# Optimization experiments

Hardware: AMD Instinct MI355X
Metric: run time of the kernel (lower is better)

Reference implementation:

```python
import jax, jax.numpy as jnp
import numpy as np

B, D, LC, LQ = 64, 128, 1024, 128
NEG = -1e30


def setup_inputs() -> dict:
    key = jax.random.key(0)
    k1, k2, k3 = jax.random.split(key, 3)
    lim = float(np.sqrt(1.0 / D))
    return {
        "C": jax.random.normal(k1, (B, D, LC), dtype=jnp.float32),
        "Q": jax.random.normal(k2, (B, D, LQ), dtype=jnp.float32),
        "cmask": jnp.ones((B, LC), dtype=jnp.float32),
        "qmask": jnp.ones((B, LQ), dtype=jnp.float32),
        "w": jax.random.uniform(k3, (3 * D,), dtype=jnp.float32, minval=-lim, maxval=lim),
    }


def reference(C, Q, cmask, qmask, w):
    # C: [B, D, Lc], Q: [B, D, Lq] -> transpose to [B, L, D] as in the torch module
    Ct = jnp.swapaxes(C, 1, 2)  # [B, Lc, D]
    Qt = jnp.swapaxes(Q, 1, 2)  # [B, Lq, D]
    d = Ct.shape[-1]
    # Trilinear decomposition of the per-step concat([Qi, C, Q*C]) . w loop:
    # S[b,c,q] = Qt[b,q] . w_q + Ct[b,c] . w_c + (Ct[b,c] * w_m) . Qt[b,q]
    w_q, w_c, w_m = w[:d], w[d:2 * d], w[2 * d:]
    s_q = Qt @ w_q                                   # [B, Lq]
    s_c = Ct @ w_c                                   # [B, Lc]
    s_m = jnp.einsum("bcd,bqd->bcq", Ct * w_m, Qt)   # [B, Lc, Lq]
    S = s_m + s_c[:, :, None] + s_q[:, None, :]      # [B, Lc, Lq]

    S1 = jax.nn.softmax(S + (1.0 - qmask)[:, None, :] * NEG, axis=2)
    S2 = jax.nn.softmax(S + (1.0 - cmask)[:, :, None] * NEG, axis=1)

    A = jnp.einsum("bcq,bqd->bcd", S1, Qt)           # [B, Lc, D]
    S12 = jnp.einsum("bcq,bkq->bck", S1, S2)         # [B, Lc, Lc]
    Bt = jnp.einsum("bck,bkd->bcd", S12, Ct)         # [B, Lc, D]

    out = jnp.concatenate([Ct, A, Ct * A, Ct * Bt], axis=2)  # [B, Lc, 4D]
    # dropout is identity in eval mode
    return jnp.swapaxes(out, 1, 2)                   # [B, 4D, Lc]
```

## Files before the change

kernel.cpp:

```cpp
#include <hip/hip_runtime.h>
#include <cstdint>
#include <cstddef>

#define B_  64
#define D_  128
#define LC_ 1024
#define LQ_ 128
#define NEGV (-1e30f)
#define NINF (-3.402823466e38f)

typedef short s16x8 __attribute__((ext_vector_type(8)));
typedef float f32x4 __attribute__((ext_vector_type(4)));

__device__ __forceinline__ unsigned short f2bf(float x) {
    union { float f; unsigned u; } v; v.f = x;
    unsigned r = v.u + 0x7fffu + ((v.u >> 16) & 1u);
    return (unsigned short)(r >> 16);
}
__device__ __forceinline__ float bf2f(unsigned short u) {
    union { unsigned u; float f; } v; v.u = ((unsigned)u) << 16; return v.f;
}

__global__ __launch_bounds__(256, 2) void k1(const float* __restrict__ C,
                                             const float* __restrict__ Q,
                                             const float* __restrict__ cmask,
                                             const float* __restrict__ qmask,
                                             const float* __restrict__ w,
                                             unsigned short* __restrict__ S1b,
                                             float* __restrict__ pmax_g,
                                             float* __restrict__ psum_g,
                                             unsigned short* __restrict__ T2pb) {
    __shared__ unsigned short CW[128 * 136];
    __shared__ unsigned short QT[128 * 136];
    __shared__ float4 red4[8][32];
    __shared__ float wc_l[128], wm_l[128], cmv_l[128], qmv_l[128], sc_l[128], sq_l[128];

    int t = threadIdx.x;
    int b = blockIdx.y, ct = blockIdx.x, c0 = ct * 128;
    int g = t >> 5, c4 = t & 31;

    float4 v[16];
    {
        const float4* Cb = (const float4*)(C + (size_t)b * D_ * LC_ + c0);
#pragma unroll
        for (int j = 0; j < 16; j++) {
            int d = j * 8 + g;
            v[j] = Cb[(size_t)d * (LC_ / 4) + c4];
        }
    }
    float* wq_l = (float*)red4;
    if (t < 128) {
        wq_l[t] = w[t];
        wc_l[t] = w[D_ + t];
        wm_l[t] = w[2 * D_ + t];
        cmv_l[t] = (1.0f - cmask[b * LC_ + c0 + t]) * NEGV;
        qmv_l[t] = (1.0f - qmask[b * LQ_ + t]) * NEGV;
    }
    __syncthreads();

    {
        float* CWf = (float*)CW;
        int qq = t >> 1, ph = t & 1;
        float sqv = 0.f;
#pragma unroll
        for (int h = 0; h < 2; h++) {
#pragma unroll
            for (int j = 0; j < 8; j++) {
                int idx = j * 256 + t;
                int r = idx >> 5, cc = idx & 31;
                float4 qv = *(const float4*)&Q[((size_t)(b * D_ + h * 64 + r)) * LQ_ + cc * 4];
                *(float4*)&CWf[r * 132 + cc * 4] = qv;
            }
            __syncthreads();
            unsigned short u[32];
#pragma unroll
            for (int k = 0; k < 32; k++) {
                float val = CWf[(ph * 32 + k) * 132 + qq];
                sqv += val * wq_l[h * 64 + ph * 32 + k];
                u[k] = f2bf(val);
            }
#pragma unroll
            for (int k4 = 0; k4 < 8; k4++) {
                ushort4 o;
                o.x = u[k4 * 4 + 0]; o.y = u[k4 * 4 + 1];
                o.z = u[k4 * 4 + 2]; o.w = u[k4 * 4 + 3];
                *(ushort4*)&QT[qq * 136 + h * 64 + ph * 32 + k4 * 4] = o;
            }
            __syncthreads();
        }
        sqv += __shfl_xor(sqv, 1, 64);
        if (ph == 0) sq_l[qq] = sqv;
    }

    {
        float4 scp = {0.f, 0.f, 0.f, 0.f};
#pragma unroll
        for (int j = 0; j < 16; j++) {
            int d = j * 8 + g;
            float wcv = wc_l[d], wmv = wm_l[d];
            scp.x += v[j].x * wcv;
            scp.y += v[j].y * wcv;
            scp.z += v[j].z * wcv;
            scp.w += v[j].w * wcv;
            ushort4 o;
            o.x = f2bf(v[j].x * wmv);
            o.y = f2bf(v[j].y * wmv);
            o.z = f2bf(v[j].z * wmv);
            o.w = f2bf(v[j].w * wmv);
            *(ushort4*)&CW[d * 136 + ((c4 ^ (j & 7)) << 2)] = o;
        }
        red4[g][c4] = scp;
    }
    __syncthreads();
    if (t < 128) {
        float s = 0.f;
#pragma unroll
        for (int gg = 0; gg < 8; gg++) {
            const float* rp = (const float*)&red4[gg][t >> 2];
            s += rp[t & 3];
        }
        sc_l[t] = s;
    }
    __syncthreads();

    int wv = t >> 6, l = t & 63, quad = l >> 4, lp = l & 15;
    int w32 = wv * 32;
    f32x4 zero = {0.f, 0.f, 0.f, 0.f};
    f32x4 acc[2][8];
#pragma unroll
    for (int mc = 0; mc < 2; mc++)
#pragma unroll
        for (int qt = 0; qt < 8; qt++) acc[mc][qt] = zero;

#pragma unroll
    for (int ks = 0; ks < 4; ks++) {
        s16x8 a[2], bb[8];
        int x3 = (ks * 4 + quad) & 7;
#pragma unroll
        for (int mc = 0; mc < 2; mc++) {
            s16x8 av;
            int c = w32 + mc * 16 + lp;
            int cb = ((c >> 2) ^ x3) << 2, clo = c & 3;
#pragma unroll
            for (int e = 0; e < 8; e++)
                av[e] = (short)CW[(ks * 32 + quad * 8 + e) * 136 + cb + clo];
            a[mc] = av;
        }
#pragma unroll
        for (int qt = 0; qt < 8; qt++)
            bb[qt] = *(const s16x8*)&QT[(qt * 16 + lp) * 136 + ks * 32 + quad * 8];
#pragma unroll
        for (int mc = 0; mc < 2; mc++)
#pragma unroll
            for (int qt = 0; qt < 8; qt++)
                acc[mc][qt] = __builtin_amdgcn_mfma_f32_16x16x32_bf16(a[mc], bb[qt], acc[mc][qt], 0, 0, 0);
    }
#pragma unroll
    for (int mc = 0; mc < 2; mc++)
#pragma unroll
        for (int qt = 0; qt < 8; qt++)
#pragma unroll
            for (int i = 0; i < 4; i++)
                acc[mc][qt][i] += sc_l[w32 + mc * 16 + quad * 4 + i] + sq_l[qt * 16 + lp];

    float qmv_r[8];
#pragma unroll
    for (int qt = 0; qt < 8; qt++) qmv_r[qt] = qmv_l[qt * 16 + lp];
    float cmv_r[2][4];
#pragma unroll
    for (int mc = 0; mc < 2; mc++)
#pragma unroll
        for (int i = 0; i < 4; i++) cmv_r[mc][i] = cmv_l[w32 + mc * 16 + quad * 4 + i];

    float rm_r[2][4];
#pragma unroll
    for (int mc = 0; mc < 2; mc++)
#pragma unroll
        for (int i = 0; i < 4; i++) {
            float m = NINF;
#pragma unroll
            for (int qt = 0; qt < 8; qt++) m = fmaxf(m, acc[mc][qt][i] + qmv_r[qt]);
#pragma unroll
            for (int off = 1; off < 16; off <<= 1) m = fmaxf(m, __shfl_xor(m, off, 64));
            rm_r[mc][i] = m;
        }

    int chunk = ct * 4 + wv;
#pragma unroll
    for (int qt = 0; qt < 8; qt++) {
        float cm = NINF;
#pragma unroll
        for (int mc = 0; mc < 2; mc++)
#pragma unroll
            for (int i = 0; i < 4; i++) cm = fmaxf(cm, acc[mc][qt][i] + cmv_r[mc][i]);
        cm = fmaxf(cm, __shfl_xor(cm, 16, 64));
        cm = fmaxf(cm, __shfl_xor(cm, 32, 64));
        float cs = 0.f;
#pragma unroll
        for (int mc = 0; mc < 2; mc++)
#pragma unroll
            for (int i = 0; i < 4; i++) cs += __expf(acc[mc][qt][i] + cmv_r[mc][i] - cm);
        cs += __shfl_xor(cs, 16, 64);
        cs += __shfl_xor(cs, 32, 64);
        if (l < 16) {
            pmax_g[((size_t)(b * 32 + chunk)) * LQ_ + qt * 16 + lp] = cm;
            psum_g[((size_t)(b * 32 + chunk)) * LQ_ + qt * 16 + lp] = cs;
        }
    }

    float ri_r[2][4], gs_r[2][4];
#pragma unroll
    for (int mc = 0; mc < 2; mc++)
#pragma unroll
        for (int i = 0; i < 4; i++) {
            float s = 0.f;
#pragma unroll
            for (int qt = 0; qt < 8; qt++) {
                float e = __expf(acc[mc][qt][i] + qmv_r[qt] - rm_r[mc][i]);
                acc[mc][qt][i] = e;
                s += e;
            }
#pragma unroll
            for (int off = 1; off < 16; off <<= 1) s += __shfl_xor(s, off, 64);
            ri_r[mc][i] = 1.0f / s;
            gs_r[mc][i] = s * __expf(rm_r[mc][i] + cmv_r[mc][i]);
        }

    __syncthreads();
#pragma unroll
    for (int mc = 0; mc < 2; mc++)
#pragma unroll
        for (int qt = 0; qt < 8; qt++)
#pragma unroll
            for (int i = 0; i < 4; i++) {
                int row = w32 + mc * 16 + quad * 4 + i;
                int q = qt * 16 + lp;
                float s1 = acc[mc][qt][i] * ri_r[mc][i];
                CW[row * 136 + q] = f2bf(s1);
                QT[q * 136 + row] = f2bf(s1 * gs_r[mc][i]);
            }
    __syncthreads();

    {
        int row = t >> 1, qh = (t & 1) * 64;
        const uint4* src = (const uint4*)&CW[row * 136 + qh];
        uint4* dst = (uint4*)&S1b[((size_t)(b * LC_ + c0 + row)) * LQ_ + qh];
#pragma unroll
        for (int j = 0; j < 8; j++) dst[j] = src[j];
    }

    f32x4 acc2[2][8];
#pragma unroll
    for (int mc = 0; mc < 2; mc++)
#pragma unroll
        for (int nt = 0; nt < 8; nt++) acc2[mc][nt] = zero;
#pragma unroll
    for (int ks = 0; ks < 4; ks++) {
        s16x8 a2[2], bb[8];
#pragma unroll
        for (int m = 0; m < 2; m++) {
            int d = w32 + m * 16 + lp;
            const float4* p = (const float4*)&C[((size_t)(b * D_ + d)) * LC_ + c0 + ks * 32 + quad * 8];
            float4 v0 = p[0], v1 = p[1];
            unsigned short* pp = (unsigned short*)&a2[m];
            pp[0] = f2bf(v0.x); pp[1] = f2bf(v0.y); pp[2] = f2bf(v0.z); pp[3] = f2bf(v0.w);
            pp[4] = f2bf(v1.x); pp[5] = f2bf(v1.y); pp[6] = f2bf(v1.z); pp[7] = f2bf(v1.w);
        }
#pragma unroll
        for (int nt = 0; nt < 8; nt++)
            bb[nt] = *(const s16x8*)&QT[(nt * 16 + lp) * 136 + ks * 32 + quad * 8];
#pragma unroll
        for (int m = 0; m < 2; m++)
#pragma unroll
            for (int nt = 0; nt < 8; nt++)
                acc2[m][nt] = __builtin_amdgcn_mfma_f32_16x16x32_bf16(a2[m], bb[nt], acc2[m][nt], 0, 0, 0);
    }
    size_t base = ((size_t)(ct * B_ + b)) * ((size_t)D_ * LQ_);
#pragma unroll
    for (int mc = 0; mc < 2; mc++)
#pragma unroll
        for (int i = 0; i < 4; i++) {
            int d = w32 + mc * 16 + quad * 4 + i;
#pragma unroll
            for (int nt = 0; nt < 8; nt++)
                T2pb[base + (size_t)d * LQ_ + nt * 16 + lp] = f2bf(acc2[mc][nt][i]);
        }
}

__global__ __launch_bounds__(256) void k2(const float* __restrict__ pmax_g,
                                          const float* __restrict__ psum_g,
                                          const unsigned short* __restrict__ T2pb,
                                          unsigned short* __restrict__ T2b) {
    __shared__ float scale_l[128];
    int t = threadIdx.x;
    int bid = blockIdx.x;
    int b = bid >> 3, dc = bid & 7;
    if (t < 128) {
        float m = NINF;
        for (int j = 0; j < 32; j++)
            m = fmaxf(m, pmax_g[((size_t)(b * 32 + j)) * LQ_ + t]);
        float s = 0.f;
        for (int j = 0; j < 32; j++)
            s += psum_g[((size_t)(b * 32 + j)) * LQ_ + t] *
                 __expf(pmax_g[((size_t)(b * 32 + j)) * LQ_ + t] - m);
        scale_l[t] = __expf(-m) / s;
    }
    __syncthreads();
    int d = dc * 16 + (t >> 4), q8 = (t & 15) * 8;
    float a8[8] = {0.f, 0.f, 0.f, 0.f, 0.f, 0.f, 0.f, 0.f};
#pragma unroll
    for (int j = 0; j < 8; j++) {
        const ushort4* p = (const ushort4*)&T2pb[(((size_t)j * B_ + b) * D_ + d) * LQ_ + q8];
        ushort4 x0 = p[0], x1 = p[1];
        a8[0] += bf2f(x0.x); a8[1] += bf2f(x0.y); a8[2] += bf2f(x0.z); a8[3] += bf2f(x0.w);
        a8[4] += bf2f(x1.x); a8[5] += bf2f(x1.y); a8[6] += bf2f(x1.z); a8[7] += bf2f(x1.w);
    }
    ushort4 o0, o1;
    o0.x = f2bf(a8[0] * scale_l[q8 + 0]);
    o0.y = f2bf(a8[1] * scale_l[q8 + 1]);
    o0.z = f2bf(a8[2] * scale_l[q8 + 2]);
    o0.w = f2bf(a8[3] * scale_l[q8 + 3]);
    o1.x = f2bf(a8[4] * scale_l[q8 + 4]);
    o1.y = f2bf(a8[5] * scale_l[q8 + 5]);
    o1.z = f2bf(a8[6] * scale_l[q8 + 6]);
    o1.w = f2bf(a8[7] * scale_l[q8 + 7]);
    size_t tb = ((size_t)(b * D_ + d)) * LQ_ + q8;
    *(ushort4*)&T2b[tb] = o0;
    *(ushort4*)&T2b[tb + 4] = o1;
}

__global__ __launch_bounds__(256) void k3(const float* __restrict__ C,
                                          const float* __restrict__ Q,
                                          const unsigned short* __restrict__ T2b,
                                          const unsigned short* __restrict__ S1b,
                                          float* __restrict__ out) {
    int t = threadIdx.x;
    int b = blockIdx.y, c0 = blockIdx.x * 128;
    int wv = t >> 6, l = t & 63, quad = l >> 4, lp = l & 15;
    int w32 = wv * 32;
    f32x4 zero = {0.f, 0.f, 0.f, 0.f};
    f32x4 accA[2][8], accB[2][8];
#pragma unroll
    for (int mc = 0; mc < 2; mc++)
#pragma unroll
        for (int nt = 0; nt < 8; nt++) { accA[mc][nt] = zero; accB[mc][nt] = zero; }

#pragma unroll
    for (int ks = 0; ks < 4; ks++) {
        s16x8 aq[2], at[2], bb[8];
#pragma unroll
        for (int mc = 0; mc < 2; mc++) {
            int d = w32 + mc * 16 + lp;
            const float4* p = (const float4*)&Q[((size_t)(b * D_ + d)) * LQ_ + ks * 32 + quad * 8];
            float4 v0 = p[0], v1 = p[1];
            unsigned short* pp = (unsigned short*)&aq[mc];
            pp[0] = f2bf(v0.x); pp[1] = f2bf(v0.y); pp[2] = f2bf(v0.z); pp[3] = f2bf(v0.w);
            pp[4] = f2bf(v1.x); pp[5] = f2bf(v1.y); pp[6] = f2bf(v1.z); pp[7] = f2bf(v1.w);
            at[mc] = *(const s16x8*)&T2b[((size_t)(b * D_ + d)) * LQ_ + ks * 32 + quad * 8];
        }
#pragma unroll
        for (int nt = 0; nt < 8; nt++)
            bb[nt] = *(const s16x8*)&S1b[((size_t)(b * LC_ + c0 + nt * 16 + lp)) * LQ_ + ks * 32 + quad * 8];
#pragma unroll
        for (int mc = 0; mc < 2; mc++)
#pragma unroll
            for (int nt = 0; nt < 8; nt++) {
                accA[mc][nt] = __builtin_amdgcn_mfma_f32_16x16x32_bf16(aq[mc], bb[nt], accA[mc][nt], 0, 0, 0);
                accB[mc][nt] = __builtin_amdgcn_mfma_f32_16x16x32_bf16(at[mc], bb[nt], accB[mc][nt], 0, 0, 0);
            }
    }
    const size_t DL = (size_t)D_ * LC_;
#pragma unroll
    for (int mc = 0; mc < 2; mc++)
#pragma unroll
        for (int i = 0; i < 4; i++) {
            int d = w32 + mc * 16 + quad * 4 + i;
            const float* Crow = C + ((size_t)(b * D_ + d)) * LC_ + c0;
            size_t ob = ((size_t)(b * 4 * D_ + d)) * LC_ + c0;
#pragma unroll
            for (int nt = 0; nt < 8; nt++) {
                int c = nt * 16 + lp;
                float cv = Crow[c];
                float a = accA[mc][nt][i];
                float bt = accB[mc][nt][i];
                out[ob + c] = cv;
                out[ob + DL + c] = a;
                out[ob + 2 * DL + c] = cv * a;
                out[ob + 3 * DL + c] = cv * bt;
            }
        }
}

extern "C" void kernel_launch(void* const* d_in, const int* in_sizes, int n_in,
                              void* d_out, int out_size, void* d_ws, size_t ws_size,
                              hipStream_t stream) {
    const float* C     = (const float*)d_in[0];
    const float* Q     = (const float*)d_in[1];
    const float* cmask = (const float*)d_in[2];
    const float* qmask = (const float*)d_in[3];
    const float* w     = (const float*)d_in[4];
    float* out = (float*)d_out;

    unsigned short* us = (unsigned short*)d_ws;
    unsigned short* S1b  = us;
    unsigned short* T2b  = S1b + (size_t)B_ * LC_ * LQ_;
    unsigned short* T2pb = T2b + (size_t)B_ * D_ * LQ_;
    float* fp = (float*)(T2pb + (size_t)8 * B_ * D_ * LQ_);
    float* pmax_g = fp;
    float* psum_g = pmax_g + (size_t)B_ * 32 * LQ_;

    k1<<<dim3(LC_ / 128, B_), 256, 0, stream>>>(C, Q, cmask, qmask, w,
                                                S1b, pmax_g, psum_g, T2pb);
    k2<<<dim3(B_ * 8), 256, 0, stream>>>(pmax_g, psum_g, T2pb, T2b);
    k3<<<dim3(LC_ / 128, B_), 256, 0, stream>>>(C, Q, T2b, S1b, out);
}
```

Baseline: 215.5 us.

## Fuse partial-T2 reduction kernel into output kernel via shared memory

Removes the separate k2 launch that reduced the eight partial T2 tiles and wrote a normalized bf16 T2 to global memory. Each k3 block now recomputes the column softmax scale and the full 128x128 T2 reduction for its batch into a padded LDS tile, then reads MFMA operands from LDS. This saves one launch and a global write/read round trip, but repeats the reduction eight times per batch (once per c-tile block). It also adds about 35 KB of LDS per block, which may lower occupancy.

```diff
diff --git a/kernel.cpp b/kernel.cpp
--- a/kernel.cpp
+++ b/kernel.cpp
@@ -287,14 +287,18 @@
         }
 }
 
-__global__ __launch_bounds__(256) void k2(const float* __restrict__ pmax_g,
+__global__ __launch_bounds__(256) void k3(const float* __restrict__ C,
+                                          const float* __restrict__ Q,
+                                          const float* __restrict__ pmax_g,
                                           const float* __restrict__ psum_g,
                                           const unsigned short* __restrict__ T2pb,
-                                          unsigned short* __restrict__ T2b) {
+                                          const unsigned short* __restrict__ S1b,
+                                          float* __restrict__ out) {
+    __shared__ unsigned short T2L[128 * 136];
     __shared__ float scale_l[128];
     int t = threadIdx.x;
-    int bid = blockIdx.x;
-    int b = bid >> 3, dc = bid & 7;
+    int b = blockIdx.y, c0 = blockIdx.x * 128;
+
     if (t < 128) {
         float m = NINF;
         for (int j = 0; j < 32; j++)
@@ -306,36 +310,34 @@
         scale_l[t] = __expf(-m) / s;
     }
     __syncthreads();
-    int d = dc * 16 + (t >> 4), q8 = (t & 15) * 8;
-    float a8[8] = {0.f, 0.f, 0.f, 0.f, 0.f, 0.f, 0.f, 0.f};
-#pragma unroll
-    for (int j = 0; j < 8; j++) {
-        const ushort4* p = (const ushort4*)&T2pb[(((size_t)j * B_ + b) * D_ + d) * LQ_ + q8];
-        ushort4 x0 = p[0], x1 = p[1];
-        a8[0] += bf2f(x0.x); a8[1] += bf2f(x0.y); a8[2] += bf2f(x0.z); a8[3] += bf2f(x0.w);
-        a8[4] += bf2f(x1.x); a8[5] += bf2f(x1.y); a8[6] += bf2f(x1.z); a8[7] += bf2f(x1.w);
-    }
-    ushort4 o0, o1;
-    o0.x = f2bf(a8[0] * scale_l[q8 + 0]);
-    o0.y = f2bf(a8[1] * scale_l[q8 + 1]);
-    o0.z = f2bf(a8[2] * scale_l[q8 + 2]);
-    o0.w = f2bf(a8[3] * scale_l[q8 + 3]);
-    o1.x = f2bf(a8[4] * scale_l[q8 + 4]);
-    o1.y = f2bf(a8[5] * scale_l[q8 + 5]);
-    o1.z = f2bf(a8[6] * scale_l[q8 + 6]);
-    o1.w = f2bf(a8[7] * scale_l[q8 + 7]);
-    size_t tb = ((size_t)(b * D_ + d)) * LQ_ + q8;
-    *(ushort4*)&T2b[tb] = o0;
-    *(ushort4*)&T2b[tb + 4] = o1;
-}
-
-__global__ __launch_bounds__(256) void k3(const float* __restrict__ C,
-                                          const float* __restrict__ Q,
-                                          const unsigned short* __restrict__ T2b,
-                                          const unsigned short* __restrict__ S1b,
-                                          float* __restrict__ out) {
-    int t = threadIdx.x;
-    int b = blockIdx.y, c0 = blockIdx.x * 128;
+
+    {
+        int dl = t >> 4, q0 = (t & 15) * 8;
+        float sc[8];
+#pragma unroll
+        for (int k = 0; k < 8; k++) sc[k] = scale_l[q0 + k];
+#pragma unroll
+        for (int dd = 0; dd < 8; dd++) {
+            int d = dd * 16 + dl;
+            float a8[8] = {0.f, 0.f, 0.f, 0.f, 0.f, 0.f, 0.f, 0.f};
+#pragma unroll
+            for (int j = 0; j < 8; j++) {
+                const ushort4* p = (const ushort4*)&T2pb[(((size_t)j * B_ + b) * D_ + d) * LQ_ + q0];
+                ushort4 x0 = p[0], x1 = p[1];
+                a8[0] += bf2f(x0.x); a8[1] += bf2f(x0.y); a8[2] += bf2f(x0.z); a8[3] += bf2f(x0.w);
+                a8[4] += bf2f(x1.x); a8[5] += bf2f(x1.y); a8[6] += bf2f(x1.z); a8[7] += bf2f(x1.w);
+            }
+            ushort4 o0, o1;
+            o0.x = f2bf(a8[0] * sc[0]); o0.y = f2bf(a8[1] * sc[1]);
+            o0.z = f2bf(a8[2] * sc[2]); o0.w = f2bf(a8[3] * sc[3]);
+            o1.x = f2bf(a8[4] * sc[4]); o1.y = f2bf(a8[5] * sc[5]);
+            o1.z = f2bf(a8[6] * sc[6]); o1.w = f2bf(a8[7] * sc[7]);
+            *(ushort4*)&T2L[d * 136 + q0] = o0;
+            *(ushort4*)&T2L[d * 136 + q0 + 4] = o1;
+        }
+    }
+    __syncthreads();
+
     int wv = t >> 6, l = t & 63, quad = l >> 4, lp = l & 15;
     int w32 = wv * 32;
     f32x4 zero = {0.f, 0.f, 0.f, 0.f};
@@ -356,7 +358,7 @@
             unsigned short* pp = (unsigned short*)&aq[mc];
             pp[0] = f2bf(v0.x); pp[1] = f2bf(v0.y); pp[2] = f2bf(v0.z); pp[3] = f2bf(v0.w);
             pp[4] = f2bf(v1.x); pp[5] = f2bf(v1.y); pp[6] = f2bf(v1.z); pp[7] = f2bf(v1.w);
-            at[mc] = *(const s16x8*)&T2b[((size_t)(b * D_ + d)) * LQ_ + ks * 32 + quad * 8];
+            at[mc] = *(const s16x8*)&T2L[d * 136 + ks * 32 + quad * 8];
         }
 #pragma unroll
         for (int nt = 0; nt < 8; nt++)
@@ -403,14 +405,13 @@
 
     unsigned short* us = (unsigned short*)d_ws;
     unsigned short* S1b  = us;
-    unsigned short* T2b  = S1b + (size_t)B_ * LC_ * LQ_;
-    unsigned short* T2pb = T2b + (size_t)B_ * D_ * LQ_;
+    unsigned short* T2pb = S1b + (size_t)B_ * LC_ * LQ_;
     float* fp = (float*)(T2pb + (size_t)8 * B_ * D_ * LQ_);
     float* pmax_g = fp;
     float* psum_g = pmax_g + (size_t)B_ * 32 * LQ_;
 
     k1<<<dim3(LC_ / 128, B_), 256, 0, stream>>>(C, Q, cmask, qmask, w,
                                                 S1b, pmax_g, psum_g, T2pb);
-    k2<<<dim3(B_ * 8), 256, 0, stream>>>(pmax_g, psum_g, T2pb, T2b);
-    k3<<<dim3(LC_ / 128, B_), 256, 0, stream>>>(C, Q, T2b, S1b, out);
+    k3<<<dim3(LC_ / 128, B_), 256, 0, stream>>>(C, Q, pmax_g, psum_g, T2pb,
+                                                S1b, out);
 }
```

Result: slower. 232.2 us (+7.8%).
